# Kernel tuning notes

Hardware: AMD Instinct MI355X
Metric: run time of the kernel (lower is better)

The kernel has to match this reference:

```python
import jax, jax.numpy as jnp
import numpy as np

HN, ND, STRIDE, ESTRIDE = 10, 40, 3, 3  # hidden_node, ndim, stride, encode_stride


def _build_graphs():
    # Dense aggregation matrices A[dst, src] equivalent to the module's fixed
    # edge lists (scatter-add of src features into dst). Graph is tiny (10/40
    # nodes) and identical across the batch, so dense matmul is the efficient
    # exact form of the gather->scatter-add.
    w = np.float32(np.exp(-(1.0 / STRIDE) ** 2))
    A_pred = np.zeros((HN, HN), np.float32)
    for j in range(HN):
        A_pred[j, j] += 1.0                      # edge [j, j], weight 1
        for dj in range(1, STRIDE - 1):          # dj = 1 only
            A_pred[(j - dj) % HN, j] += w        # edge [j, j-dj]
            A_pred[(j + dj) % HN, j] += w        # edge [j, j+dj]
    A_enc = np.zeros((HN, ND), np.float32)
    A_dec = np.zeros((ND, HN), np.float32)
    for j in range(HN):
        cg = (j * ND // HN) % ND                 # center_grid = 4j
        for i in range(cg - ESTRIDE, cg + ESTRIDE):
            A_enc[j, i % ND] += 1.0              # grid i -> hidden j
            A_dec[i % ND, j] += 1.0              # hidden j -> grid i
    return jnp.asarray(A_enc), jnp.asarray(A_pred), jnp.asarray(A_dec)

A_ENC, A_PRED, A_DEC = _build_graphs()


def setup_inputs() -> dict:
    key = jax.random.key(0)
    ks = jax.random.split(key, 12)
    B, HF = 524288, 8
    s = 0.3  # modest weight scale
    return {
        "x": jax.random.normal(ks[0], (B, ND), jnp.float32),
        "z": jax.random.uniform(ks[1], (B, HN, HF), dtype=jnp.float32),
        "y": jax.random.uniform(ks[2], (B, ND, 1), dtype=jnp.float32),
        "enc_rel_w": jax.random.normal(ks[3], (HF, 1), jnp.float32) * s,
        "enc_rel_b": jax.random.normal(ks[4], (HF,), jnp.float32) * s,
        "enc_root_w": jax.random.normal(ks[5], (HF, HF), jnp.float32) * s,
        "pred_rel_w": jax.random.normal(ks[6], (HF, HF), jnp.float32) * s,
        "pred_rel_b": jax.random.normal(ks[7], (HF,), jnp.float32) * s,
        "pred_root_w": jax.random.normal(ks[8], (HF, HF), jnp.float32) * s,
        "dec_rel_w": jax.random.normal(ks[9], (1, HF), jnp.float32) * s,
        "dec_rel_b": jax.random.normal(ks[10], (1,), jnp.float32) * s,
        "dec_root_w": jax.random.normal(ks[11], (1, 1), jnp.float32) * s,
    }


def reference(x, z, y, enc_rel_w, enc_rel_b, enc_root_w,
              pred_rel_w, pred_rel_b, pred_root_w,
              dec_rel_w, dec_rel_b, dec_root_w):
    xb = x[..., None]  # [B, 40, 1]
    # encoder GraphConv((1, 8) -> 8): lin_rel(agg(x_src)) + lin_root(z)
    agg = jnp.einsum('ds,bsf->bdf', A_ENC, xb)                 # [B, 10, 1]
    z1 = jax.nn.relu(agg @ enc_rel_w.T + enc_rel_b + z @ enc_root_w.T)
    # predictor GraphConv(8 -> 8) with edge weights folded into A_PRED
    agg2 = jnp.einsum('ds,bsf->bdf', A_PRED, z1)               # [B, 10, 8]
    z2 = jax.nn.relu(agg2 @ pred_rel_w.T + pred_rel_b + z1 @ pred_root_w.T)
    # decoder GraphConv((8, 1) -> 1)
    agg3 = jnp.einsum('ds,bsf->bdf', A_DEC, z2)                # [B, 40, 8]
    out = agg3 @ dec_rel_w.T + dec_rel_b + y @ dec_root_w.T   # [B, 40, 1]
    return out[..., 0]                                         # [B, 40]
```

## Files before the change

kernel.cpp:

```cpp
#include <hip/hip_runtime.h>


#define HN 10
#define ND 40
#define HF 8
#define TPB 256

__global__ __launch_bounds__(TPB) void gnn_kernel(
    const float* __restrict__ x,
    const float* __restrict__ z,
    const float* __restrict__ y,
    const float* __restrict__ enc_rel_w,
    const float* __restrict__ enc_rel_b,
    const float* __restrict__ enc_root_w,
    const float* __restrict__ pred_rel_w,
    const float* __restrict__ pred_rel_b,
    const float* __restrict__ pred_root_w,
    const float* __restrict__ dec_rel_w,
    const float* __restrict__ dec_rel_b,
    const float* __restrict__ dec_root_w,
    float* __restrict__ out,
    int B)
{
    const long long e = (long long)blockIdx.x * TPB + threadIdx.x;

    const float w = 0.8948393168143698f;

    const float4* xr = (const float4*)(x + e * ND);
    const float4* zr = (const float4*)(z + e * (HN * HF));
    const float4* yr = (const float4*)(y + e * ND);
    float4*       og = (float4*)(out + e * ND);

    const float drb   = dec_rel_b[0];
    const float droot = dec_root_w[0];

    auto enc_row = [&](float aggv, float4 v0, float4 v1, float (&r)[HF]) {
        float zrow[HF] = {v0.x, v0.y, v0.z, v0.w, v1.x, v1.y, v1.z, v1.w};
        #pragma unroll
        for (int f = 0; f < HF; ++f) {
            float acc = aggv * enc_rel_w[f] + enc_rel_b[f];
            #pragma unroll
            for (int g = 0; g < HF; ++g)
                acc += zrow[g] * enc_root_w[f * HF + g];
            r[f] = fmaxf(acc, 0.0f);
        }
    };

    auto emit = [&](const float (&rm)[HF], const float (&rc)[HF],
                    const float (&rp)[HF]) -> float {
        float a2[HF];
        #pragma unroll
        for (int f = 0; f < HF; ++f)
            a2[f] = rc[f] + w * (rm[f] + rp[f]);
        float s = 0.0f;
        #pragma unroll
        for (int f = 0; f < HF; ++f) {
            float acc = pred_rel_b[f];
            #pragma unroll
            for (int g = 0; g < HF; ++g)
                acc += a2[g] * pred_rel_w[f * HF + g];
            #pragma unroll
            for (int g = 0; g < HF; ++g)
                acc += rc[g] * pred_root_w[f * HF + g];
            s += fmaxf(acc, 0.0f) * dec_rel_w[f];
        }
        return s;
    };

    auto store_out = [&](int idx, float sa, float sb, float4 yv) {
        const float pair = sa + sb + drb;
        float4 o;
        o.x = (sa + drb) + yv.x * droot;
        o.y = pair       + yv.y * droot;
        o.z = pair       + yv.z * droot;
        o.w = (sb + drb) + yv.w * droot;
        og[idx] = o;
    };

    float4 X0 = xr[0], X1 = xr[1], X2 = xr[2], X3 = xr[3], X4 = xr[4],
           X5 = xr[5], X6 = xr[6], X7 = xr[7], X8 = xr[8], X9 = xr[9];
    const float a0 = X9.y + X9.z + X9.w + X0.x + X0.y + X0.z;
    const float a1 = X0.y + X0.z + X0.w + X1.x + X1.y + X1.z;
    const float a2v= X1.y + X1.z + X1.w + X2.x + X2.y + X2.z;
    const float a3 = X2.y + X2.z + X2.w + X3.x + X3.y + X3.z;
    const float a4 = X3.y + X3.z + X3.w + X4.x + X4.y + X4.z;
    const float a5 = X4.y + X4.z + X4.w + X5.x + X5.y + X5.z;
    const float a6 = X5.y + X5.z + X5.w + X6.x + X6.y + X6.z;
    const float a7 = X6.y + X6.z + X6.w + X7.x + X7.y + X7.z;
    const float a8 = X7.y + X7.z + X7.w + X8.x + X8.y + X8.z;
    const float a9 = X8.y + X8.z + X8.w + X9.x + X9.y + X9.z;

    float u0 = a2v, u1 = a3, u2 = a4, u3 = a5,
          u4 = a6,  u5 = a7, u6 = a8, u7 = a9;

    {
    }
    float r0s[HF], r1s[HF];
    {
        float4 zq0 = zr[0], zq1 = zr[1], zq2 = zr[2], zq3 = zr[3];
        enc_row(a0, zq0, zq1, r0s);
        enc_row(a1, zq2, zq3, r1s);
    }

    float rm[HF], rc[HF];
    #pragma unroll
    for (int f = 0; f < HF; ++f) { rm[f] = r0s[f]; rc[f] = r1s[f]; }

    float t0 = 0.f, t1 = 0.f, t2 = 0.f, t3 = 0.f,
          t4 = 0.f, t5 = 0.f, t6 = 0.f, t7 = 0.f;

    #pragma unroll 1
    for (int j = 1; j <= 4; ++j) {
        float4 q0 = zr[4*j + 0], q1 = zr[4*j + 1],
               q2 = zr[4*j + 2], q3 = zr[4*j + 3];

        float rp0[HF], rp1[HF];
        enc_row(u0, q0, q1, rp0);
        enc_row(u1, q2, q3, rp1);

        const float sA = emit(rm, rc, rp0);
        const float sB = emit(rc, rp0, rp1);

        t0 = t2; t1 = t3; t2 = t4; t3 = t5; t4 = t6; t5 = t7;
        t6 = sA; t7 = sB;
        u0 = u2; u1 = u3; u2 = u4; u3 = u5; u4 = u6; u5 = u7;
        #pragma unroll
        for (int f = 0; f < HF; ++f) { rm[f] = rp0[f]; rc[f] = rp1[f]; }
    }

    float4 Y0 = yr[0], Y1 = yr[1], Y2 = yr[2], Y3 = yr[3], Y4 = yr[4],
           Y5 = yr[5], Y6 = yr[6], Y7 = yr[7], Y8 = yr[8], Y9 = yr[9];

    const float s9 = emit(rm, rc, r0s);
    const float s0 = emit(rc, r0s, r1s);

    store_out(0, s0, t0, Y0);
    store_out(1, t0, t1, Y1);
    store_out(2, t1, t2, Y2);
    store_out(3, t2, t3, Y3);
    store_out(4, t3, t4, Y4);
    store_out(5, t4, t5, Y5);
    store_out(6, t5, t6, Y6);
    store_out(7, t6, t7, Y7);
    store_out(8, t7, s9, Y8);
    store_out(9, s9, s0, Y9);
}

extern "C" void kernel_launch(void* const* d_in, const int* in_sizes, int n_in,
                              void* d_out, int out_size, void* d_ws, size_t ws_size,
                              hipStream_t stream) {
    const float* x          = (const float*)d_in[0];
    const float* z          = (const float*)d_in[1];
    const float* y          = (const float*)d_in[2];
    const float* enc_rel_w  = (const float*)d_in[3];
    const float* enc_rel_b  = (const float*)d_in[4];
    const float* enc_root_w = (const float*)d_in[5];
    const float* pred_rel_w = (const float*)d_in[6];
    const float* pred_rel_b = (const float*)d_in[7];
    const float* pred_root_w= (const float*)d_in[8];
    const float* dec_rel_w  = (const float*)d_in[9];
    const float* dec_rel_b  = (const float*)d_in[10];
    const float* dec_root_w = (const float*)d_in[11];
    float* out = (float*)d_out;

    const int B = in_sizes[0] / ND;
    const int blocks = B / TPB;
    gnn_kernel<<<blocks, TPB, 0, stream>>>(
        x, z, y, enc_rel_w, enc_rel_b, enc_root_w,
        pred_rel_w, pred_rel_b, pred_root_w,
        dec_rel_w, dec_rel_b, dec_root_w, out, B);
}
```

Baseline: 398.1 us.

## Stage x, z, y and out through per-wave LDS for coalesced global access

Each wave now loads its 64 rows of x, z and y with lane-contiguous float4 accesses. It transposes x, z and the output through padded per-wave LDS buffers so every thread still works on its own row. The previous layout had each thread reading a separate 160- or 320-byte row, which gives strided, poorly coalesced accesses. z chunks are double-buffered in LDS with the next global load issued ahead of compute. The change adds LDS traffic and relies on hand-placed waitcnt and sched barriers with no __syncthreads, assuming the lanes of a wave stay in lockstep.

```diff
diff --git a/kernel.cpp b/kernel.cpp
--- a/kernel.cpp
+++ b/kernel.cpp
@@ -5,6 +5,9 @@
 #define ND 40
 #define HF 8
 #define TPB 256
+#define WLEN 64
+#define ROW4 11
+#define ZROW 5
 
 __global__ __launch_bounds__(TPB) void gnn_kernel(
     const float* __restrict__ x,
@@ -22,14 +25,19 @@
     float* __restrict__ out,
     int B)
 {
-    const long long e = (long long)blockIdx.x * TPB + threadIdx.x;
+    __shared__ float4 lds4[TPB * ROW4];
+    const int t  = threadIdx.x;
+    const int l  = t & 63;
+    const int wv = t >> 6;
+    const long long W = (long long)blockIdx.x * TPB + wv * WLEN;
+    float4* wl = lds4 + wv * (WLEN * ROW4);
 
     const float w = 0.8948393168143698f;
 
-    const float4* xr = (const float4*)(x + e * ND);
-    const float4* zr = (const float4*)(z + e * (HN * HF));
-    const float4* yr = (const float4*)(y + e * ND);
-    float4*       og = (float4*)(out + e * ND);
+    const float4* xg4 = (const float4*)x;
+    const float4* zg4 = (const float4*)z;
+    const float4* yg4 = (const float4*)y;
+    float4*       og4 = (float4*)out;
 
     const float drb   = dec_rel_b[0];
     const float droot = dec_root_w[0];
@@ -67,41 +75,61 @@
         return s;
     };
 
-    auto store_out = [&](int idx, float sa, float sb, float4 yv) {
-        const float pair = sa + sb + drb;
-        float4 o;
-        o.x = (sa + drb) + yv.x * droot;
-        o.y = pair       + yv.y * droot;
-        o.z = pair       + yv.z * droot;
-        o.w = (sb + drb) + yv.w * droot;
-        og[idx] = o;
-    };
-
-    float4 X0 = xr[0], X1 = xr[1], X2 = xr[2], X3 = xr[3], X4 = xr[4],
-           X5 = xr[5], X6 = xr[6], X7 = xr[7], X8 = xr[8], X9 = xr[9];
-    const float a0 = X9.y + X9.z + X9.w + X0.x + X0.y + X0.z;
-    const float a1 = X0.y + X0.z + X0.w + X1.x + X1.y + X1.z;
-    const float a2v= X1.y + X1.z + X1.w + X2.x + X2.y + X2.z;
-    const float a3 = X2.y + X2.z + X2.w + X3.x + X3.y + X3.z;
-    const float a4 = X3.y + X3.z + X3.w + X4.x + X4.y + X4.z;
-    const float a5 = X4.y + X4.z + X4.w + X5.x + X5.y + X5.z;
-    const float a6 = X5.y + X5.z + X5.w + X6.x + X6.y + X6.z;
-    const float a7 = X6.y + X6.z + X6.w + X7.x + X7.y + X7.z;
-    const float a8 = X7.y + X7.z + X7.w + X8.x + X8.y + X8.z;
-    const float a9 = X8.y + X8.z + X8.w + X9.x + X9.y + X9.z;
+    float4 xv4[10];
+    #pragma unroll
+    for (int k = 0; k < 10; ++k) xv4[k] = xg4[W * 10 + l + 64 * k];
+    float4 zt[4];
+    #pragma unroll
+    for (int k = 0; k < 4; ++k) {
+        int i = l + 64 * k; int r = i >> 2, m = i & 3;
+        zt[k] = zg4[(W + r) * 20 + m];
+    }
+    #pragma unroll
+    for (int k = 0; k < 10; ++k) {
+        int i = l + 64 * k; int r = i / 10, q = i - r * 10;
+        wl[r * ROW4 + q] = xv4[k];
+    }
+    asm volatile("s_waitcnt lgkmcnt(0)" ::: "memory");
+    __builtin_amdgcn_sched_barrier(0);
+    float xv[ND];
+    #pragma unroll
+    for (int k = 0; k < 10; ++k) {
+        float4 v = wl[l * ROW4 + k];
+        xv[4*k] = v.x; xv[4*k+1] = v.y; xv[4*k+2] = v.z; xv[4*k+3] = v.w;
+    }
+    const float a0 = xv[37] + xv[38] + xv[39] + xv[0] + xv[1] + xv[2];
+    const float a1 = xv[1]  + xv[2]  + xv[3]  + xv[4] + xv[5] + xv[6];
+    const float a2v= xv[5]  + xv[6]  + xv[7]  + xv[8] + xv[9] + xv[10];
+    const float a3 = xv[9]  + xv[10] + xv[11] + xv[12]+ xv[13]+ xv[14];
+    const float a4 = xv[13] + xv[14] + xv[15] + xv[16]+ xv[17]+ xv[18];
+    const float a5 = xv[17] + xv[18] + xv[19] + xv[20]+ xv[21]+ xv[22];
+    const float a6 = xv[21] + xv[22] + xv[23] + xv[24]+ xv[25]+ xv[26];
+    const float a7 = xv[25] + xv[26] + xv[27] + xv[28]+ xv[29]+ xv[30];
+    const float a8 = xv[29] + xv[30] + xv[31] + xv[32]+ xv[33]+ xv[34];
+    const float a9 = xv[33] + xv[34] + xv[35] + xv[36]+ xv[37]+ xv[38];
 
     float u0 = a2v, u1 = a3, u2 = a4, u3 = a5,
           u4 = a6,  u5 = a7, u6 = a8, u7 = a9;
 
-    {
-    }
+    #pragma unroll
+    for (int k = 0; k < 4; ++k) {
+        int i = l + 64 * k; int r = i >> 2, m = i & 3;
+        wl[r * ZROW + m] = zt[k];
+    }
+    #pragma unroll
+    for (int k = 0; k < 4; ++k) {
+        int i = l + 64 * k; int r = i >> 2, m = i & 3;
+        zt[k] = zg4[(W + r) * 20 + 4 + m];
+    }
+    asm volatile("s_waitcnt lgkmcnt(0)" ::: "memory");
+    __builtin_amdgcn_sched_barrier(0);
     float r0s[HF], r1s[HF];
     {
-        float4 zq0 = zr[0], zq1 = zr[1], zq2 = zr[2], zq3 = zr[3];
-        enc_row(a0, zq0, zq1, r0s);
-        enc_row(a1, zq2, zq3, r1s);
-    }
-
+        float4 q0 = wl[l * ZROW + 0], q1 = wl[l * ZROW + 1],
+               q2 = wl[l * ZROW + 2], q3 = wl[l * ZROW + 3];
+        enc_row(a0, q0, q1, r0s);
+        enc_row(a1, q2, q3, r1s);
+    }
     float rm[HF], rc[HF];
     #pragma unroll
     for (int f = 0; f < HF; ++f) { rm[f] = r0s[f]; rc[f] = r1s[f]; }
@@ -111,13 +139,27 @@
 
     #pragma unroll 1
     for (int j = 1; j <= 4; ++j) {
-        float4 q0 = zr[4*j + 0], q1 = zr[4*j + 1],
-               q2 = zr[4*j + 2], q3 = zr[4*j + 3];
+        float4* bw = wl + (j & 1) * (WLEN * ZROW);
+        #pragma unroll
+        for (int k = 0; k < 4; ++k) {
+            int i = l + 64 * k; int r = i >> 2, m = i & 3;
+            bw[r * ZROW + m] = zt[k];
+        }
+        if (j < 4) {
+            #pragma unroll
+            for (int k = 0; k < 4; ++k) {
+                int i = l + 64 * k; int r = i >> 2, m = i & 3;
+                zt[k] = zg4[(W + r) * 20 + 4 * (j + 1) + m];
+            }
+        }
+        asm volatile("s_waitcnt lgkmcnt(0)" ::: "memory");
+        __builtin_amdgcn_sched_barrier(0);
+        float4 q0 = bw[l * ZROW + 0], q1 = bw[l * ZROW + 1],
+               q2 = bw[l * ZROW + 2], q3 = bw[l * ZROW + 3];
 
         float rp0[HF], rp1[HF];
         enc_row(u0, q0, q1, rp0);
         enc_row(u1, q2, q3, rp1);
-
         const float sA = emit(rm, rc, rp0);
         const float sB = emit(rc, rp0, rp1);
 
@@ -128,22 +170,42 @@
         for (int f = 0; f < HF; ++f) { rm[f] = rp0[f]; rc[f] = rp1[f]; }
     }
 
-    float4 Y0 = yr[0], Y1 = yr[1], Y2 = yr[2], Y3 = yr[3], Y4 = yr[4],
-           Y5 = yr[5], Y6 = yr[6], Y7 = yr[7], Y8 = yr[8], Y9 = yr[9];
+    float4 yv4[10];
+    #pragma unroll
+    for (int k = 0; k < 10; ++k) yv4[k] = yg4[W * 10 + l + 64 * k];
 
     const float s9 = emit(rm, rc, r0s);
     const float s0 = emit(rc, r0s, r1s);
 
-    store_out(0, s0, t0, Y0);
-    store_out(1, t0, t1, Y1);
-    store_out(2, t1, t2, Y2);
-    store_out(3, t2, t3, Y3);
-    store_out(4, t3, t4, Y4);
-    store_out(5, t4, t5, Y5);
-    store_out(6, t5, t6, Y6);
-    store_out(7, t6, t7, Y7);
-    store_out(8, t7, s9, Y8);
-    store_out(9, s9, s0, Y9);
+    asm volatile("s_waitcnt lgkmcnt(0)" ::: "memory");
+    __builtin_amdgcn_sched_barrier(0);
+    {
+        float sa[10] = {s0, t0, t1, t2, t3, t4, t5, t6, t7, s9};
+        float sb[10] = {t0, t1, t2, t3, t4, t5, t6, t7, s9, s0};
+        #pragma unroll
+        for (int k = 0; k < 10; ++k) {
+            const float pair = sa[k] + sb[k] + drb;
+            float4 vo;
+            vo.x = sa[k] + drb;
+            vo.y = pair;
+            vo.z = pair;
+            vo.w = sb[k] + drb;
+            wl[l * ROW4 + k] = vo;
+        }
+    }
+    asm volatile("s_waitcnt lgkmcnt(0)" ::: "memory");
+    __builtin_amdgcn_sched_barrier(0);
+    #pragma unroll
+    for (int k = 0; k < 10; ++k) {
+        int i = l + 64 * k; int e2 = i / 10, q = i - e2 * 10;
+        float4 p = wl[e2 * ROW4 + q];
+        float4 vy = yv4[k];
+        p.x += vy.x * droot;
+        p.y += vy.y * droot;
+        p.z += vy.z * droot;
+        p.w += vy.w * droot;
+        og4[W * 10 + i] = p;
+    }
 }
 
 extern "C" void kernel_launch(void* const* d_in, const int* in_sizes, int n_in,
```

Result: no change. 398.8 us (+0.2%).

## Issue all x/z loads upfront via inline asm with staged vmcnt waits

Applied to the files above, without the earlier changes.

Replaces the rolled loop of per-iteration z loads with a fully unrolled pipeline. All x and z dwordx4 loads are issued at kernel start through inline-asm global_load, and s_waitcnt vmcnt is staged so each encoder stage waits only for its own data. The y loads are issued before the last two emits so their latency overlaps compute. The aim is more memory-level parallelism for a bandwidth-bound kernel, at the cost of many more live VGPRs (30 float4s) and therefore possibly lower occupancy.

```diff
diff --git a/kernel.cpp b/kernel.cpp
--- a/kernel.cpp
+++ b/kernel.cpp
@@ -5,6 +5,12 @@
 #define ND 40
 #define HF 8
 #define TPB 256
+
+#define GLD(dst, addr) \
+    asm volatile("global_load_dwordx4 %0, %1, off" : "=v"(dst) : "v"(addr))
+#define VMWAIT(n) do { \
+    asm volatile("s_waitcnt vmcnt(" #n ")"); \
+    __builtin_amdgcn_sched_barrier(0); } while (0)
 
 __global__ __launch_bounds__(TPB) void gnn_kernel(
     const float* __restrict__ x,
@@ -30,6 +36,18 @@
     const float4* zr = (const float4*)(z + e * (HN * HF));
     const float4* yr = (const float4*)(y + e * ND);
     float4*       og = (float4*)(out + e * ND);
+
+    float4 X0, X1, X2, X3, X4, X5, X6, X7, X8, X9;
+    GLD(X0, xr + 0); GLD(X1, xr + 1); GLD(X2, xr + 2); GLD(X3, xr + 3);
+    GLD(X4, xr + 4); GLD(X5, xr + 5); GLD(X6, xr + 6); GLD(X7, xr + 7);
+    GLD(X8, xr + 8); GLD(X9, xr + 9);
+    float4 Z0, Z1, Z2, Z3, Z4, Z5, Z6, Z7, Z8, Z9,
+           Z10, Z11, Z12, Z13, Z14, Z15, Z16, Z17, Z18, Z19;
+    GLD(Z0,  zr +  0); GLD(Z1,  zr +  1); GLD(Z2,  zr +  2); GLD(Z3,  zr +  3);
+    GLD(Z4,  zr +  4); GLD(Z5,  zr +  5); GLD(Z6,  zr +  6); GLD(Z7,  zr +  7);
+    GLD(Z8,  zr +  8); GLD(Z9,  zr +  9); GLD(Z10, zr + 10); GLD(Z11, zr + 11);
+    GLD(Z12, zr + 12); GLD(Z13, zr + 13); GLD(Z14, zr + 14); GLD(Z15, zr + 15);
+    GLD(Z16, zr + 16); GLD(Z17, zr + 17); GLD(Z18, zr + 18); GLD(Z19, zr + 19);
 
     const float drb   = dec_rel_b[0];
     const float droot = dec_root_w[0];
@@ -77,8 +95,7 @@
         og[idx] = o;
     };
 
-    float4 X0 = xr[0], X1 = xr[1], X2 = xr[2], X3 = xr[3], X4 = xr[4],
-           X5 = xr[5], X6 = xr[6], X7 = xr[7], X8 = xr[8], X9 = xr[9];
+    VMWAIT(20);
     const float a0 = X9.y + X9.z + X9.w + X0.x + X0.y + X0.z;
     const float a1 = X0.y + X0.z + X0.w + X1.x + X1.y + X1.z;
     const float a2v= X1.y + X1.z + X1.w + X2.x + X2.y + X2.z;
@@ -90,59 +107,57 @@
     const float a8 = X7.y + X7.z + X7.w + X8.x + X8.y + X8.z;
     const float a9 = X8.y + X8.z + X8.w + X9.x + X9.y + X9.z;
 
-    float u0 = a2v, u1 = a3, u2 = a4, u3 = a5,
-          u4 = a6,  u5 = a7, u6 = a8, u7 = a9;
+    VMWAIT(16);
+    float r0[HF], r1[HF];
+    enc_row(a0, Z0, Z1, r0);
+    enc_row(a1, Z2, Z3, r1);
 
-    {
-    }
-    float r0s[HF], r1s[HF];
-    {
-        float4 zq0 = zr[0], zq1 = zr[1], zq2 = zr[2], zq3 = zr[3];
-        enc_row(a0, zq0, zq1, r0s);
-        enc_row(a1, zq2, zq3, r1s);
-    }
+    VMWAIT(12);
+    float r2[HF], r3[HF];
+    enc_row(a2v, Z4, Z5, r2);
+    enc_row(a3,  Z6, Z7, r3);
+    const float s1 = emit(r0, r1, r2);
+    const float s2 = emit(r1, r2, r3);
 
-    float rm[HF], rc[HF];
-    #pragma unroll
-    for (int f = 0; f < HF; ++f) { rm[f] = r0s[f]; rc[f] = r1s[f]; }
+    VMWAIT(8);
+    float r4[HF], r5[HF];
+    enc_row(a4, Z8,  Z9,  r4);
+    enc_row(a5, Z10, Z11, r5);
+    const float s3 = emit(r2, r3, r4);
+    const float s4 = emit(r3, r4, r5);
 
-    float t0 = 0.f, t1 = 0.f, t2 = 0.f, t3 = 0.f,
-          t4 = 0.f, t5 = 0.f, t6 = 0.f, t7 = 0.f;
+    VMWAIT(4);
+    float r6[HF], r7[HF];
+    enc_row(a6, Z12, Z13, r6);
+    enc_row(a7, Z14, Z15, r7);
+    const float s5 = emit(r4, r5, r6);
+    const float s6 = emit(r5, r6, r7);
 
-    #pragma unroll 1
-    for (int j = 1; j <= 4; ++j) {
-        float4 q0 = zr[4*j + 0], q1 = zr[4*j + 1],
-               q2 = zr[4*j + 2], q3 = zr[4*j + 3];
+    VMWAIT(0);
+    float r8[HF], r9[HF];
+    enc_row(a8, Z16, Z17, r8);
+    enc_row(a9, Z18, Z19, r9);
+    const float s7 = emit(r6, r7, r8);
+    const float s8 = emit(r7, r8, r9);
 
-        float rp0[HF], rp1[HF];
-        enc_row(u0, q0, q1, rp0);
-        enc_row(u1, q2, q3, rp1);
+    float4 Y0, Y1, Y2, Y3, Y4, Y5, Y6, Y7, Y8, Y9;
+    GLD(Y0, yr + 0); GLD(Y1, yr + 1); GLD(Y2, yr + 2); GLD(Y3, yr + 3);
+    GLD(Y4, yr + 4); GLD(Y5, yr + 5); GLD(Y6, yr + 6); GLD(Y7, yr + 7);
+    GLD(Y8, yr + 8); GLD(Y9, yr + 9);
 
-        const float sA = emit(rm, rc, rp0);
-        const float sB = emit(rc, rp0, rp1);
+    const float s9 = emit(r8, r9, r0);
+    const float s0 = emit(r9, r0, r1);
 
-        t0 = t2; t1 = t3; t2 = t4; t3 = t5; t4 = t6; t5 = t7;
-        t6 = sA; t7 = sB;
-        u0 = u2; u1 = u3; u2 = u4; u3 = u5; u4 = u6; u5 = u7;
-        #pragma unroll
-        for (int f = 0; f < HF; ++f) { rm[f] = rp0[f]; rc[f] = rp1[f]; }
-    }
-
-    float4 Y0 = yr[0], Y1 = yr[1], Y2 = yr[2], Y3 = yr[3], Y4 = yr[4],
-           Y5 = yr[5], Y6 = yr[6], Y7 = yr[7], Y8 = yr[8], Y9 = yr[9];
-
-    const float s9 = emit(rm, rc, r0s);
-    const float s0 = emit(rc, r0s, r1s);
-
-    store_out(0, s0, t0, Y0);
-    store_out(1, t0, t1, Y1);
-    store_out(2, t1, t2, Y2);
-    store_out(3, t2, t3, Y3);
-    store_out(4, t3, t4, Y4);
-    store_out(5, t4, t5, Y5);
-    store_out(6, t5, t6, Y6);
-    store_out(7, t6, t7, Y7);
-    store_out(8, t7, s9, Y8);
+    VMWAIT(0);
+    store_out(0, s0, s1, Y0);
+    store_out(1, s1, s2, Y1);
+    store_out(2, s2, s3, Y2);
+    store_out(3, s3, s4, Y3);
+    store_out(4, s4, s5, Y4);
+    store_out(5, s5, s6, Y5);
+    store_out(6, s6, s7, Y6);
+    store_out(7, s7, s8, Y7);
+    store_out(8, s8, s9, Y8);
     store_out(9, s9, s0, Y9);
 }
 
```

New measurement: 413.8 us. 1.04x slower.
